# Optimization experiments

Measured on AMD Instinct MI355X. Metric: run time of the kernel, lower is better.

The kernel has to match this reference:

```python
import jax, jax.numpy as jnp
import numpy as np

# OpenCV fixed separable Gaussian kernel for ksize=3, sigma=0 (getGaussianKernel small-kernel table)
GAUSS_1D = jnp.array([0.25, 0.5, 0.25], dtype=jnp.float32)
# OpenCV Laplacian kernel for ksize=3 (Sobel dxx + dyy aperture 3)
LAP_K = jnp.array([[2.0, 0.0, 2.0], [0.0, -8.0, 0.0], [2.0, 0.0, 2.0]], dtype=jnp.float32)


def _depthwise_conv(img, kernel2d):
    # img: (N, H, W); kernel2d: (kh, kw). BORDER_REFLECT_101 == jnp.pad mode='reflect'.
    kh, kw = kernel2d.shape
    ph, pw = kh // 2, kw // 2
    padded = jnp.pad(img, ((0, 0), (ph, ph), (pw, pw)), mode='reflect')
    out = jax.lax.conv_general_dilated(
        padded[:, None, :, :], kernel2d[None, None, :, :],
        window_strides=(1, 1), padding='VALID')
    return out[:, 0]


def setup_inputs() -> dict:
    key = jax.random.key(0)
    x = jax.random.uniform(key, (32, 3, 512, 512), dtype=jnp.float32)
    return {"x": x}


def reference(x):
    B, C, H, W = x.shape
    img = x.reshape(B * C, H, W)
    # src = clip(x*255, 0, 255).astype('uint8')  -> truncation toward zero (values >= 0, so floor)
    src = jnp.floor(jnp.clip(img * 255.0, 0.0, 255.0))
    # cv2.GaussianBlur(ksize=3, sigma=0): separable [1,2,1]/4 kernel, rounded back to uint8
    g2d = GAUSS_1D[:, None] * GAUSS_1D[None, :]
    blurred = jnp.clip(jnp.round(_depthwise_conv(src, g2d)), 0.0, 255.0)
    # cv2.Laplacian(CV_16S, ksize=3): integer-exact on integer-valued input
    lap = _depthwise_conv(blurred, LAP_K)
    # cv2.convertScaleAbs: saturate_cast<uchar>(|dst|)
    abs_dst = jnp.clip(jnp.round(jnp.abs(lap)), 0.0, 255.0)
    return abs_dst.reshape(B, C, H, W)
```

## Files before the change

### kernel.cpp

```cpp
#include <hip/hip_runtime.h>
#include <math.h>

#define IMG_H 512
#define IMG_W 512
#define TW 256
#define TH 32
#define SRC_ROWS 36
#define SRC_SLOTS 66

__device__ __forceinline__ int reflect101(int i, int n) {
    if (i < 0) i = -i;
    if (i >= n) i = 2 * n - 2 - i;
    return i;
}

__device__ __forceinline__ unsigned int quant(float v) {
    return (unsigned int)floorf(fminf(fmaxf(v * 255.0f, 0.0f), 255.0f));
}

#define UNPACK(row, F) do {                                                   \
    unsigned int u0_ = s_src[row][cx];                                        \
    unsigned int u1_ = s_src[row][cx + 1];                                    \
    unsigned int u2_ = s_src[row][cx + 2];                                    \
    F##0 = (float)((u0_ >> 16) & 0xffu);                                      \
    F##1 = (float)(u0_ >> 24);                                                \
    F##2 = (float)(u1_ & 0xffu);                                              \
    F##3 = (float)((u1_ >> 8) & 0xffu);                                       \
    F##4 = (float)((u1_ >> 16) & 0xffu);                                      \
    F##5 = (float)(u1_ >> 24);                                                \
    F##6 = (float)(u2_ & 0xffu);                                              \
    F##7 = (float)((u2_ >> 8) & 0xffu);                                       \
} while (0)

#define BLUR(A, B, C, BL) do {                                                \
    float c0_ = A##0 + 2.0f * B##0 + C##0;                                    \
    float c1_ = A##1 + 2.0f * B##1 + C##1;                                    \
    float c2_ = A##2 + 2.0f * B##2 + C##2;                                    \
    float c3_ = A##3 + 2.0f * B##3 + C##3;                                    \
    float c4_ = A##4 + 2.0f * B##4 + C##4;                                    \
    float c5_ = A##5 + 2.0f * B##5 + C##5;                                    \
    float c6_ = A##6 + 2.0f * B##6 + C##6;                                    \
    float c7_ = A##7 + 2.0f * B##7 + C##7;                                    \
    BL##0 = rintf((c0_ + 2.0f * c1_ + c2_) * 0.0625f);                        \
    BL##1 = rintf((c1_ + 2.0f * c2_ + c3_) * 0.0625f);                        \
    BL##2 = rintf((c2_ + 2.0f * c3_ + c4_) * 0.0625f);                        \
    BL##3 = rintf((c3_ + 2.0f * c4_ + c5_) * 0.0625f);                        \
    BL##4 = rintf((c4_ + 2.0f * c5_ + c6_) * 0.0625f);                        \
    BL##5 = rintf((c5_ + 2.0f * c6_ + c7_) * 0.0625f);                        \
} while (0)

#define LAP_STORE(BM, B0, BP, yy) do {                                        \
    float4 o_;                                                                \
    float h_;                                                                 \
    h_ = (BM##0 + BM##2 + BP##0 + BP##2) - 4.0f * B0##1;                      \
    o_.x = fminf(2.0f * fabsf(h_), 255.0f);                                   \
    h_ = (BM##1 + BM##3 + BP##1 + BP##3) - 4.0f * B0##2;                      \
    o_.y = fminf(2.0f * fabsf(h_), 255.0f);                                   \
    h_ = (BM##2 + BM##4 + BP##2 + BP##4) - 4.0f * B0##3;                      \
    o_.z = fminf(2.0f * fabsf(h_), 255.0f);                                   \
    h_ = (BM##3 + BM##5 + BP##3 + BP##5) - 4.0f * B0##4;                      \
    o_.w = fminf(2.0f * fabsf(h_), 255.0f);                                   \
    *(float4*)&op[(size_t)(ty0 + (yy)) * IMG_W + xo] = o_;                    \
} while (0)

__global__ __launch_bounds__(256, 4) void lap_fused(const float* __restrict__ in,
                                                    float* __restrict__ out) {
    __shared__ unsigned int s_src[SRC_ROWS][SRC_SLOTS];

    const int img = blockIdx.z;
    const int ty0 = blockIdx.y * TH;
    const int tx0 = blockIdx.x * TW;
    const float* __restrict__ ip = in + (size_t)img * (IMG_H * IMG_W);
    float* __restrict__ op = out + (size_t)img * (IMG_H * IMG_W);
    const int tid = threadIdx.x;

    for (int i = tid; i < SRC_ROWS * SRC_SLOTS; i += 256) {
        int r = i / SRC_SLOTS;
        int j = i - r * SRC_SLOTS;
        int gy = reflect101(ty0 + r - 2, IMG_H);
        int gx0 = tx0 - 4 + 4 * j;
        const float* rowp = ip + (size_t)gy * IMG_W;
        float4 v;
        if (gx0 >= 0 && gx0 + 3 < IMG_W) {
            v = *(const float4*)(rowp + gx0);
        } else {
            float* pv = (float*)&v;
            #pragma unroll
            for (int k = 0; k < 4; ++k) pv[k] = rowp[reflect101(gx0 + k, IMG_W)];
        }
        s_src[r][j] = quant(v.x) | (quant(v.y) << 8) | (quant(v.z) << 16) | (quant(v.w) << 24);
    }
    __syncthreads();

    const int cx = tid & 63;
    const int rw = tid >> 6;
    const int xo = tx0 + 4 * cx;
    const int lr0 = 8 * rw;

    float sA0, sA1, sA2, sA3, sA4, sA5, sA6, sA7;
    float sB0, sB1, sB2, sB3, sB4, sB5, sB6, sB7;
    float sC0, sC1, sC2, sC3, sC4, sC5, sC6, sC7;
    float bP0, bP1, bP2, bP3, bP4, bP5;
    float bQ0, bQ1, bQ2, bQ3, bQ4, bQ5;
    float bR0, bR1, bR2, bR3, bR4, bR5;

    UNPACK(lr0 + 0, sA);
    UNPACK(lr0 + 1, sB);
    UNPACK(lr0 + 2, sC);
    BLUR(sA, sB, sC, bP);
    UNPACK(lr0 + 3, sA);
    BLUR(sB, sC, sA, bQ);

    const int yb = 8 * rw;
    UNPACK(lr0 + 4, sB);  BLUR(sC, sA, sB, bR);  LAP_STORE(bP, bQ, bR, yb + 0);
    UNPACK(lr0 + 5, sC);  BLUR(sA, sB, sC, bP);  LAP_STORE(bQ, bR, bP, yb + 1);
    UNPACK(lr0 + 6, sA);  BLUR(sB, sC, sA, bQ);  LAP_STORE(bR, bP, bQ, yb + 2);
    UNPACK(lr0 + 7, sB);  BLUR(sC, sA, sB, bR);  LAP_STORE(bP, bQ, bR, yb + 3);
    UNPACK(lr0 + 8, sC);  BLUR(sA, sB, sC, bP);  LAP_STORE(bQ, bR, bP, yb + 4);
    UNPACK(lr0 + 9, sA);  BLUR(sB, sC, sA, bQ);  LAP_STORE(bR, bP, bQ, yb + 5);
    UNPACK(lr0 + 10, sB); BLUR(sC, sA, sB, bR);  LAP_STORE(bP, bQ, bR, yb + 6);
    UNPACK(lr0 + 11, sC); BLUR(sA, sB, sC, bP);  LAP_STORE(bQ, bR, bP, yb + 7);
}

extern "C" void kernel_launch(void* const* d_in, const int* in_sizes, int n_in,
                              void* d_out, int out_size, void* d_ws, size_t ws_size,
                              hipStream_t stream) {
    const float* x = (const float*)d_in[0];
    float* out = (float*)d_out;
    dim3 grid(IMG_W / TW, IMG_H / TH, 96);
    dim3 block(256);
    lap_fused<<<grid, block, 0, stream>>>(x, out);
}
```

Baseline: 45.94 us.

## Enlarge tile height and compute eight output columns per thread

Tile height doubles to 64 rows, so the reflected halo rows are a smaller share of each tile. Each thread now produces 8 columns instead of 4, which cuts redundant shared-memory reads and horizontal blur work per output pixel. It also reads shared memory with uint2 loads and writes output with nontemporal stores. Quantisation drops the max-with-zero clamp, relying on inputs being non-negative, and the larger tile halves the grid and raises register use, which could lower occupancy.

Measured after the change: 55.85 us. 1.22x slower.

```diff
diff --git a/kernel.cpp b/kernel.cpp
--- a/kernel.cpp
+++ b/kernel.cpp
@@ -4,9 +4,11 @@
 #define IMG_H 512
 #define IMG_W 512
 #define TW 256
-#define TH 32
-#define SRC_ROWS 36
+#define TH 64
+#define SRC_ROWS 68
 #define SRC_SLOTS 66
+
+typedef float f32x4 __attribute__((ext_vector_type(4)));
 
 __device__ __forceinline__ int reflect101(int i, int n) {
     if (i < 0) i = -i;
@@ -14,53 +16,78 @@
     return i;
 }
 
-__device__ __forceinline__ unsigned int quant(float v) {
-    return (unsigned int)floorf(fminf(fmaxf(v * 255.0f, 0.0f), 255.0f));
+__device__ __forceinline__ unsigned int quant4(float4 v) {
+    unsigned int a = (unsigned int)fminf(v.x * 255.0f, 255.0f);
+    unsigned int b = (unsigned int)fminf(v.y * 255.0f, 255.0f);
+    unsigned int c = (unsigned int)fminf(v.z * 255.0f, 255.0f);
+    unsigned int d = (unsigned int)fminf(v.w * 255.0f, 255.0f);
+    return a | (b << 8) | (c << 16) | (d << 24);
 }
 
-#define UNPACK(row, F) do {                                                   \
-    unsigned int u0_ = s_src[row][cx];                                        \
-    unsigned int u1_ = s_src[row][cx + 1];                                    \
-    unsigned int u2_ = s_src[row][cx + 2];                                    \
-    F##0 = (float)((u0_ >> 16) & 0xffu);                                      \
-    F##1 = (float)(u0_ >> 24);                                                \
-    F##2 = (float)(u1_ & 0xffu);                                              \
-    F##3 = (float)((u1_ >> 8) & 0xffu);                                       \
-    F##4 = (float)((u1_ >> 16) & 0xffu);                                      \
-    F##5 = (float)(u1_ >> 24);                                                \
-    F##6 = (float)(u2_ & 0xffu);                                              \
-    F##7 = (float)((u2_ >> 8) & 0xffu);                                       \
+#define UNPACK(lr, F) do {                                                    \
+    uint2 ua_ = *(const uint2*)&s_src[lr][sb];                                \
+    uint2 ub_ = *(const uint2*)&s_src[lr][sb + 2];                            \
+    F##0  = (float)((ua_.x >> 16) & 0xffu);                                   \
+    F##1  = (float)(ua_.x >> 24);                                             \
+    F##2  = (float)(ua_.y & 0xffu);                                           \
+    F##3  = (float)((ua_.y >> 8) & 0xffu);                                    \
+    F##4  = (float)((ua_.y >> 16) & 0xffu);                                   \
+    F##5  = (float)(ua_.y >> 24);                                             \
+    F##6  = (float)(ub_.x & 0xffu);                                           \
+    F##7  = (float)((ub_.x >> 8) & 0xffu);                                    \
+    F##8  = (float)((ub_.x >> 16) & 0xffu);                                   \
+    F##9  = (float)(ub_.x >> 24);                                             \
+    F##10 = (float)(ub_.y & 0xffu);                                           \
+    F##11 = (float)((ub_.y >> 8) & 0xffu);                                    \
 } while (0)
 
 #define BLUR(A, B, C, BL) do {                                                \
-    float c0_ = A##0 + 2.0f * B##0 + C##0;                                    \
-    float c1_ = A##1 + 2.0f * B##1 + C##1;                                    \
-    float c2_ = A##2 + 2.0f * B##2 + C##2;                                    \
-    float c3_ = A##3 + 2.0f * B##3 + C##3;                                    \
-    float c4_ = A##4 + 2.0f * B##4 + C##4;                                    \
-    float c5_ = A##5 + 2.0f * B##5 + C##5;                                    \
-    float c6_ = A##6 + 2.0f * B##6 + C##6;                                    \
-    float c7_ = A##7 + 2.0f * B##7 + C##7;                                    \
+    float c0_  = A##0  + 2.0f * B##0  + C##0;                                 \
+    float c1_  = A##1  + 2.0f * B##1  + C##1;                                 \
+    float c2_  = A##2  + 2.0f * B##2  + C##2;                                 \
+    float c3_  = A##3  + 2.0f * B##3  + C##3;                                 \
+    float c4_  = A##4  + 2.0f * B##4  + C##4;                                 \
+    float c5_  = A##5  + 2.0f * B##5  + C##5;                                 \
+    float c6_  = A##6  + 2.0f * B##6  + C##6;                                 \
+    float c7_  = A##7  + 2.0f * B##7  + C##7;                                 \
+    float c8_  = A##8  + 2.0f * B##8  + C##8;                                 \
+    float c9_  = A##9  + 2.0f * B##9  + C##9;                                 \
+    float c10_ = A##10 + 2.0f * B##10 + C##10;                                \
+    float c11_ = A##11 + 2.0f * B##11 + C##11;                                \
     BL##0 = rintf((c0_ + 2.0f * c1_ + c2_) * 0.0625f);                        \
     BL##1 = rintf((c1_ + 2.0f * c2_ + c3_) * 0.0625f);                        \
     BL##2 = rintf((c2_ + 2.0f * c3_ + c4_) * 0.0625f);                        \
     BL##3 = rintf((c3_ + 2.0f * c4_ + c5_) * 0.0625f);                        \
     BL##4 = rintf((c4_ + 2.0f * c5_ + c6_) * 0.0625f);                        \
     BL##5 = rintf((c5_ + 2.0f * c6_ + c7_) * 0.0625f);                        \
+    BL##6 = rintf((c6_ + 2.0f * c7_ + c8_) * 0.0625f);                        \
+    BL##7 = rintf((c7_ + 2.0f * c8_ + c9_) * 0.0625f);                        \
+    BL##8 = rintf((c8_ + 2.0f * c9_ + c10_) * 0.0625f);                       \
+    BL##9 = rintf((c9_ + 2.0f * c10_ + c11_) * 0.0625f);                      \
 } while (0)
 
 #define LAP_STORE(BM, B0, BP, yy) do {                                        \
-    float4 o_;                                                                \
+    f32x4 o0_, o1_;                                                           \
     float h_;                                                                 \
     h_ = (BM##0 + BM##2 + BP##0 + BP##2) - 4.0f * B0##1;                      \
-    o_.x = fminf(2.0f * fabsf(h_), 255.0f);                                   \
+    o0_.x = fminf(2.0f * fabsf(h_), 255.0f);                                  \
     h_ = (BM##1 + BM##3 + BP##1 + BP##3) - 4.0f * B0##2;                      \
-    o_.y = fminf(2.0f * fabsf(h_), 255.0f);                                   \
+    o0_.y = fminf(2.0f * fabsf(h_), 255.0f);                                  \
     h_ = (BM##2 + BM##4 + BP##2 + BP##4) - 4.0f * B0##3;                      \
-    o_.z = fminf(2.0f * fabsf(h_), 255.0f);                                   \
+    o0_.z = fminf(2.0f * fabsf(h_), 255.0f);                                  \
     h_ = (BM##3 + BM##5 + BP##3 + BP##5) - 4.0f * B0##4;                      \
-    o_.w = fminf(2.0f * fabsf(h_), 255.0f);                                   \
-    *(float4*)&op[(size_t)(ty0 + (yy)) * IMG_W + xo] = o_;                    \
+    o0_.w = fminf(2.0f * fabsf(h_), 255.0f);                                  \
+    h_ = (BM##4 + BM##6 + BP##4 + BP##6) - 4.0f * B0##5;                      \
+    o1_.x = fminf(2.0f * fabsf(h_), 255.0f);                                  \
+    h_ = (BM##5 + BM##7 + BP##5 + BP##7) - 4.0f * B0##6;                      \
+    o1_.y = fminf(2.0f * fabsf(h_), 255.0f);                                  \
+    h_ = (BM##6 + BM##8 + BP##6 + BP##8) - 4.0f * B0##7;                      \
+    o1_.z = fminf(2.0f * fabsf(h_), 255.0f);                                  \
+    h_ = (BM##7 + BM##9 + BP##7 + BP##9) - 4.0f * B0##8;                      \
+    o1_.w = fminf(2.0f * fabsf(h_), 255.0f);                                  \
+    float* orow_ = &op[(size_t)(ty0 + (yy)) * IMG_W + xo];                    \
+    __builtin_nontemporal_store(o0_, (f32x4*)orow_);                          \
+    __builtin_nontemporal_store(o1_, (f32x4*)(orow_ + 4));                    \
 } while (0)
 
 __global__ __launch_bounds__(256, 4) void lap_fused(const float* __restrict__ in,
@@ -88,21 +115,23 @@
             #pragma unroll
             for (int k = 0; k < 4; ++k) pv[k] = rowp[reflect101(gx0 + k, IMG_W)];
         }
-        s_src[r][j] = quant(v.x) | (quant(v.y) << 8) | (quant(v.z) << 16) | (quant(v.w) << 24);
+        s_src[r][j] = quant4(v);
     }
     __syncthreads();
 
-    const int cx = tid & 63;
-    const int rw = tid >> 6;
-    const int xo = tx0 + 4 * cx;
-    const int lr0 = 8 * rw;
+    const int cg = tid & 31;
+    const int rb = tid >> 5;
+    const int xo = tx0 + 8 * cg;
+    const int sb = 2 * cg;
+    const int lr0 = 8 * rb;
+    const int yb = 8 * rb;
 
-    float sA0, sA1, sA2, sA3, sA4, sA5, sA6, sA7;
-    float sB0, sB1, sB2, sB3, sB4, sB5, sB6, sB7;
-    float sC0, sC1, sC2, sC3, sC4, sC5, sC6, sC7;
-    float bP0, bP1, bP2, bP3, bP4, bP5;
-    float bQ0, bQ1, bQ2, bQ3, bQ4, bQ5;
-    float bR0, bR1, bR2, bR3, bR4, bR5;
+    float sA0, sA1, sA2, sA3, sA4, sA5, sA6, sA7, sA8, sA9, sA10, sA11;
+    float sB0, sB1, sB2, sB3, sB4, sB5, sB6, sB7, sB8, sB9, sB10, sB11;
+    float sC0, sC1, sC2, sC3, sC4, sC5, sC6, sC7, sC8, sC9, sC10, sC11;
+    float bP0, bP1, bP2, bP3, bP4, bP5, bP6, bP7, bP8, bP9;
+    float bQ0, bQ1, bQ2, bQ3, bQ4, bQ5, bQ6, bQ7, bQ8, bQ9;
+    float bR0, bR1, bR2, bR3, bR4, bR5, bR6, bR7, bR8, bR9;
 
     UNPACK(lr0 + 0, sA);
     UNPACK(lr0 + 1, sB);
@@ -111,7 +140,6 @@
     UNPACK(lr0 + 3, sA);
     BLUR(sB, sC, sA, bQ);
 
-    const int yb = 8 * rw;
     UNPACK(lr0 + 4, sB);  BLUR(sC, sA, sB, bR);  LAP_STORE(bP, bQ, bR, yb + 0);
     UNPACK(lr0 + 5, sC);  BLUR(sA, sB, sC, bP);  LAP_STORE(bQ, bR, bP, yb + 1);
     UNPACK(lr0 + 6, sA);  BLUR(sB, sC, sA, bQ);  LAP_STORE(bR, bP, bQ, yb + 2);
```
